# Performance work log

Measured on AMD Instinct MI355X. Metric: run time of the kernel, lower is better.

The kernel has to match this reference:

```python
import jax, jax.numpy as jnp
import numpy as np

EPS = 1e-6
ROPE_THETA = 10000.0
NUM_HEADS = 32
NUM_KV_HEADS = 8
HEAD_DIM = 128
HIDDEN = 4096
B, S = 2, 2048


def setup_inputs() -> dict:
    key = jax.random.key(0)
    ks = jax.random.split(key, 6)
    scale = 0.02
    return {
        "hidden_states": jax.random.normal(ks[0], (B, S, HIDDEN), dtype=jnp.float32),
        "position_ids": jnp.arange(S, dtype=jnp.int64 if jax.config.jax_enable_x64 else jnp.int32)[None, :],
        "Wq": jax.random.normal(ks[1], (HIDDEN, NUM_HEADS * HEAD_DIM), dtype=jnp.float32) * scale,
        "Wk": jax.random.normal(ks[2], (HIDDEN, NUM_KV_HEADS * HEAD_DIM), dtype=jnp.float32) * scale,
        "Wv": jax.random.normal(ks[3], (HIDDEN, NUM_KV_HEADS * HEAD_DIM), dtype=jnp.float32) * scale,
        "Wo": jax.random.normal(ks[4], (NUM_HEADS * HEAD_DIM, HIDDEN), dtype=jnp.float32) * scale,
        "q_norm_w": jnp.ones((HEAD_DIM,), dtype=jnp.float32),
        "k_norm_w": jnp.ones((HEAD_DIM,), dtype=jnp.float32),
    }


def _rms_norm(x, w):
    # RMSNorm over last dim (head_dim)
    var = jnp.mean(jnp.square(x), axis=-1, keepdims=True)
    return x * jax.lax.rsqrt(var + EPS) * w


def _rope(x, position_ids):
    # x: [B, H, S, D]; Llama-style half-split rotation
    d = x.shape[-1]
    inv_freq = 1.0 / (ROPE_THETA ** (jnp.arange(0, d, 2, dtype=jnp.float32) / d))  # [D/2]
    ang = position_ids[:, :, None].astype(jnp.float32) * inv_freq[None, None, :]   # [B, S, D/2]
    emb = jnp.concatenate([ang, ang], axis=-1)                                     # [B, S, D]
    cos = jnp.cos(emb)[:, None, :, :]
    sin = jnp.sin(emb)[:, None, :, :]
    x1, x2 = x[..., : d // 2], x[..., d // 2:]
    rot = jnp.concatenate([-x2, x1], axis=-1)
    return x * cos + rot * sin


def reference(hidden_states, position_ids, Wq, Wk, Wv, Wo, q_norm_w, k_norm_w):
    b, s, _ = hidden_states.shape
    q = (hidden_states @ Wq).reshape(b, s, NUM_HEADS, HEAD_DIM).transpose(0, 2, 1, 3)
    k = (hidden_states @ Wk).reshape(b, s, NUM_KV_HEADS, HEAD_DIM).transpose(0, 2, 1, 3)
    v = (hidden_states @ Wv).reshape(b, s, NUM_KV_HEADS, HEAD_DIM).transpose(0, 2, 1, 3)

    q = _rms_norm(q, q_norm_w)
    k = _rms_norm(k, k_norm_w)

    q = _rope(q, position_ids)
    k = _rope(k, position_ids)

    groups = NUM_HEADS // NUM_KV_HEADS
    k = jnp.repeat(k, groups, axis=1)  # repeat_interleave along head dim
    v = jnp.repeat(v, groups, axis=1)

    scale = 1.0 / jnp.sqrt(jnp.float32(HEAD_DIM))
    scores = jnp.einsum("bhqd,bhkd->bhqk", q, k) * scale
    causal = jnp.tril(jnp.ones((s, s), dtype=bool))
    scores = jnp.where(causal[None, None], scores, jnp.finfo(scores.dtype).min)
    attn = jax.nn.softmax(scores, axis=-1)
    out = jnp.einsum("bhqk,bhkd->bhqd", attn, v)
    out = out.transpose(0, 2, 1, 3).reshape(b, s, NUM_HEADS * HEAD_DIM)
    return out @ Wo
```

## Files before the change

kernel.cpp:

```cpp
#include <hip/hip_runtime.h>
#include <stdint.h>
#include <stddef.h>

#define S_LEN 2048
#define BATCH 2
#define NHEADS 32
#define NKV 8
#define HD 128
#define HIDDEN 4096
#define T_TOK (BATCH * S_LEN)
#define QKV_W 6144

typedef unsigned short u16;
typedef __attribute__((ext_vector_type(4))) float f32x4;
typedef __attribute__((ext_vector_type(16))) float f32x16;
typedef __attribute__((ext_vector_type(8))) short s16x8;
typedef __attribute__((ext_vector_type(4))) unsigned short u16x4;
typedef __attribute__((ext_vector_type(4))) unsigned int u32x4;

__device__ __forceinline__ u16 f2bf(float f) {
  unsigned int u = __builtin_bit_cast(unsigned int, f);
  unsigned int r = (u + 0x7FFFu + ((u >> 16) & 1u)) >> 16;
  return (u16)r;
}
__device__ __forceinline__ float bf2f(u16 h) {
  return __builtin_bit_cast(float, ((unsigned int)h) << 16);
}

__device__ __forceinline__ void gload16(const void* g, void* l) {
  __builtin_amdgcn_global_load_lds((__attribute__((address_space(1))) void*)g,
                                   (__attribute__((address_space(3))) void*)l,
                                   16, 0, 0);
}

__device__ __forceinline__ unsigned cvtpk(float a, float b) {
  unsigned r;
  asm("v_cvt_pk_bf16_f32 %0, %1, %2" : "=v"(r) : "v"(a), "v"(b));
  return r;
}
__device__ __forceinline__ void lohi_dup(unsigned W, unsigned& lo, unsigned& hi) {
  unsigned a = W, b = W;
  asm volatile("v_permlane32_swap_b32 %0, %1" : "+v"(a), "+v"(b));
  lo = a; hi = b;
}

__global__ __launch_bounds__(256) void k_convert(const float* __restrict__ in,
                                                 u16* __restrict__ out, int n8) {
  int i = blockIdx.x * 256 + threadIdx.x;
  if (i >= n8) return;
  float4 a = ((const float4*)in)[i * 2];
  float4 b = ((const float4*)in)[i * 2 + 1];
  u16x4 lo = {f2bf(a.x), f2bf(a.y), f2bf(a.z), f2bf(a.w)};
  u16x4 hi = {f2bf(b.x), f2bf(b.y), f2bf(b.z), f2bf(b.w)};
  ((u16x4*)out)[i * 2] = lo;
  ((u16x4*)out)[i * 2 + 1] = hi;
}

__global__ __launch_bounds__(256) void k_transpose_w(const float* __restrict__ W,
                                                     u16* __restrict__ Wt, int K,
                                                     int N, int outRowOff,
                                                     int outStride) {
  __shared__ float tl[32][33];
  int k0 = blockIdx.x * 32, n0 = blockIdx.y * 32;
  int t = threadIdx.x;
  int r = t >> 3, c4 = (t & 7) * 4;
  float4 v = *(const float4*)&W[(size_t)(k0 + r) * N + n0 + c4];
  tl[r][c4] = v.x; tl[r][c4 + 1] = v.y; tl[r][c4 + 2] = v.z; tl[r][c4 + 3] = v.w;
  __syncthreads();
  u16x4 o = {f2bf(tl[c4][r]), f2bf(tl[c4 + 1][r]), f2bf(tl[c4 + 2][r]),
             f2bf(tl[c4 + 3][r])};
  *(u16x4*)&Wt[(size_t)(outRowOff + n0 + r) * outStride + k0 + c4] = o;
}

__global__ __launch_bounds__(256) void k_rope_tab(const int* __restrict__ pos,
                                                  float* __restrict__ tab) {
  int i = blockIdx.x * 256 + threadIdx.x;
  int s = i >> 6, l = i & 63;
  float p = (float)pos[s];
  float ang = p * expf(-(float)l * 0.14391156516342163f);
  tab[s * 128 + l] = cosf(ang);
  tab[s * 128 + 64 + l] = sinf(ang);
}

template <typename OutT>
__global__ __launch_bounds__(256, 2) void k_gemm128(const u16* __restrict__ A,
                                                    const u16* __restrict__ Bt,
                                                    OutT* __restrict__ C,
                                                    int N, int K) {
  __shared__ u16 As[2][8192];
  __shared__ u16 Bs[2][8192];
  int nbn = N >> 7;
  int nwg = gridDim.x;
  int orig = blockIdx.x;
  int q8 = nwg >> 3, r8 = nwg & 7;
  int xcd = orig & 7, sub = orig >> 3;
  int wgid = (xcd < r8 ? xcd * (q8 + 1) : r8 * (q8 + 1) + (xcd - r8) * q8) + sub;
  int bm = wgid / nbn, bn = wgid % nbn;
  int tid = threadIdx.x, wid = tid >> 6, lane = tid & 63;
  int wm = wid >> 1, wn = wid & 1;
  int g = lane >> 4, c = lane & 15;
  int l3 = lane >> 3, l7 = lane & 7;
  int swz = c & 7;
  int xunit = (l7 ^ l3) * 8;

  f32x4 acc[4][4];
#pragma unroll
  for (int m = 0; m < 4; m++)
#pragma unroll
    for (int n = 0; n < 4; n++) acc[m][n] = (f32x4){0.f, 0.f, 0.f, 0.f};

  const u16* aBase = A + (size_t)(bm * 128 + wid * 32 + l3) * K + xunit;
  const u16* bBase = Bt + (size_t)(bn * 128 + wid * 32 + l3) * K + xunit;

  auto stgA = [&](int buf, int j, size_t koff) {
    gload16(aBase + (size_t)(j * 8) * K + koff, &As[buf][(wid * 32 + j * 8) * 64]);
  };
  auto stgB = [&](int buf, int j, size_t koff) {
    gload16(bBase + (size_t)(j * 8) * K + koff, &Bs[buf][(wid * 32 + j * 8) * 64]);
  };

  int nt = K >> 6;
#pragma unroll
  for (int j = 0; j < 4; j++) { stgA(0, j, 0); stgB(0, j, 0); }
  __syncthreads();

  for (int t = 0; t < nt; t++) {
    int cb = t & 1;
    const u16* Ab = &As[cb][0];
    const u16* Bb = &Bs[cb][0];
    bool s1 = (t + 1 < nt);
    size_t k1 = (size_t)(t + 1) << 6;

    s16x8 af[4][2], bf[4][2];
#pragma unroll
    for (int mi = 0; mi < 4; mi++)
#pragma unroll
      for (int ks = 0; ks < 2; ks++)
        af[mi][ks] = *(const s16x8*)&Ab[(wm * 64 + mi * 16 + c) * 64 +
                                        (((ks * 4 + g) ^ swz) * 8)];
#pragma unroll
    for (int nj = 0; nj < 4; nj++)
#pragma unroll
      for (int ks = 0; ks < 2; ks++)
        bf[nj][ks] = *(const s16x8*)&Bb[(wn * 64 + nj * 16 + c) * 64 +
                                        (((ks * 4 + g) ^ swz) * 8)];
    if (s1) {
#pragma unroll
      for (int j = 0; j < 4; j++) { stgA(cb ^ 1, j, k1); stgB(cb ^ 1, j, k1); }
    }
    __builtin_amdgcn_s_setprio(1);
#pragma unroll
    for (int mi = 0; mi < 4; mi++)
#pragma unroll
      for (int nj = 0; nj < 4; nj++)
#pragma unroll
        for (int ks = 0; ks < 2; ks++)
          acc[mi][nj] = __builtin_amdgcn_mfma_f32_16x16x32_bf16(
              af[mi][ks], bf[nj][ks], acc[mi][nj], 0, 0, 0);
    __builtin_amdgcn_s_setprio(0);
    __syncthreads();
  }

#pragma unroll
  for (int m = 0; m < 4; m++)
#pragma unroll
    for (int n = 0; n < 4; n++) {
      size_t row = (size_t)bm * 128 + wm * 64 + m * 16 + g * 4;
      size_t col = (size_t)bn * 128 + wn * 64 + n * 16 + c;
#pragma unroll
      for (int r = 0; r < 4; r++) {
        float v = acc[m][n][r];
        if constexpr (sizeof(OutT) == 2)
          C[(row + r) * N + col] = (OutT)f2bf(v);
        else
          C[(row + r) * N + col] = (OutT)v;
      }
    }
}

__global__ __launch_bounds__(256) void k_rmsrope(u16* __restrict__ QK,
                                                 const float* __restrict__ w,
                                                 const float* __restrict__ tab,
                                                 int H, int rowStride) {
  int row = blockIdx.x * 4 + (threadIdx.x >> 6);
  int lane = threadIdx.x & 63;
  int t = row / H, h = row - t * H;
  int s = t & (S_LEN - 1);
  u16* p = QK + (size_t)t * rowStride + h * HD;
  float x1 = bf2f(p[lane]), x2 = bf2f(p[lane + 64]);
  float ss = x1 * x1 + x2 * x2;
#pragma unroll
  for (int o = 32; o >= 1; o >>= 1) ss += __shfl_xor(ss, o);
  float inv = rsqrtf(ss * (1.0f / 128.0f) + 1e-6f);
  float y1 = x1 * inv * w[lane], y2 = x2 * inv * w[lane + 64];
  float cs = tab[s * 128 + lane], sn = tab[s * 128 + 64 + lane];
  p[lane] = f2bf(y1 * cs - y2 * sn);
  p[lane + 64] = f2bf(y2 * cs + y1 * sn);
}

__global__ __launch_bounds__(256) void k_transpose_v(const u16* __restrict__ QKV,
                                                     u16* __restrict__ Vt) {
  __shared__ u16 tl[32][40];
  int bkh = blockIdx.x;
  int s0 = blockIdx.y * 32, d0 = blockIdx.z * 32;
  int b = bkh >> 3, kh = bkh & 7;
  int t = threadIdx.x, r = t >> 3, c4 = (t & 7) * 4;
  const u16* src =
      QKV + (size_t)(b * S_LEN + s0 + r) * QKV_W + 5120 + kh * HD + d0 + c4;
  u16x4 v = *(const u16x4*)src;
  tl[r][c4] = v[0]; tl[r][c4 + 1] = v[1]; tl[r][c4 + 2] = v[2]; tl[r][c4 + 3] = v[3];
  __syncthreads();
  u16x4 o = {tl[c4][r], tl[c4 + 1][r], tl[c4 + 2][r], tl[c4 + 3][r]};
  *(u16x4*)&Vt[(size_t)(bkh * HD + d0 + r) * S_LEN + s0 + c4] = o;
}

__global__ __launch_bounds__(256) void k_attn(const u16* __restrict__ QKV,
                                              const u16* __restrict__ Vt,
                                              u16* __restrict__ Oact) {
  __shared__ u16 Ks[2][64 * 128];
  __shared__ u16 Vs[2][128 * 64];
  int bid = blockIdx.x;
  int xcd = bid & 7, slot = bid >> 3;
  int grp = xcd * 2 + (slot >> 5);
  int b = grp >> 3, kh = grp & 7;
  int s32 = slot & 31;
  int pr = s32 >> 2;
  int h = kh * 4 + (s32 & 3);
  int w = threadIdx.x >> 6, lane = threadIdx.x & 63;
  int q31 = lane & 31, hh = lane >> 5;
  const float qscale = 0.12751740810f;

  const char* Kg = (const char*)(QKV + (size_t)b * S_LEN * QKV_W + 4096 + kh * HD);
  const char* Vg = (const char*)(Vt + (size_t)(b * 8 + kh) * HD * S_LEN);

#pragma unroll 1
  for (int half = 0; half < 2; half++) {
    __syncthreads();
    int qt = half ? 15 - pr : pr;
    int qw0 = qt * 128 + w * 32;

    s16x8 qf[8];
    const u16* Qp = QKV + (size_t)(b * S_LEN + qw0 + q31) * QKV_W + h * HD + hh * 8;
#pragma unroll
    for (int dc = 0; dc < 8; dc++) {
      s16x8 raw = *(const s16x8*)(Qp + dc * 16);
#pragma unroll
      for (int e = 0; e < 8; e++)
        qf[dc][e] = (short)f2bf(bf2f((u16)raw[e]) * qscale);
    }

    f32x16 o[4];
#pragma unroll
    for (int d = 0; d < 4; d++)
#pragma unroll
      for (int r = 0; r < 16; r++) o[d][r] = 0.f;
    float m = -3.0e38f, l = 0.f;

    int nch = 2 * qt + 2;

    {
      char* KsB = (char*)Ks[0];
      char* VsB = (char*)Vs[0];
#pragma unroll
      for (int j = 0; j < 4; j++) {
        int ins = w * 4 + j;
        int row = ins * 4 + (lane >> 4);
        int bc = ((lane & 15) * 16) ^ ((row & 7) << 4);
        gload16(Kg + (size_t)row * 12288 + bc, KsB + ins * 1024);
      }
#pragma unroll
      for (int j = 0; j < 4; j++) {
        int ins = w * 4 + j;
        int row = ins * 8 + (lane >> 3);
        int bc = ((lane & 7) * 16) ^ ((row & 7) << 4);
        gload16(Vg + (size_t)row * 4096 + bc, VsB + ins * 1024);
      }
    }

    int cur = 0;
    for (int ch = 0; ch < nch; ch++) {
      int kb = ch * 64;
      __syncthreads();
      if (ch + 1 < nch) {
        char* KsB = (char*)Ks[cur ^ 1];
        char* VsB = (char*)Vs[cur ^ 1];
        int kb2 = kb + 64;
#pragma unroll
        for (int j = 0; j < 4; j++) {
          int ins = w * 4 + j;
          int row = ins * 4 + (lane >> 4);
          int bc = ((lane & 15) * 16) ^ ((row & 7) << 4);
          gload16(Kg + (size_t)(kb2 + row) * 12288 + bc, KsB + ins * 1024);
        }
#pragma unroll
        for (int j = 0; j < 4; j++) {
          int ins = w * 4 + j;
          int row = ins * 8 + (lane >> 3);
          int bc = ((lane & 7) * 16) ^ ((row & 7) << 4);
          gload16(Vg + (size_t)row * 4096 + (size_t)kb2 * 2 + bc, VsB + ins * 1024);
        }
      }
      if (kb <= qw0 + 31) {
        char* KsB = (char*)Ks[cur];
        char* VsB = (char*)Vs[cur];
        f32x16 sA, sB;
#pragma unroll
        for (int r = 0; r < 16; r++) { sA[r] = 0.f; sB[r] = 0.f; }
        int sw = (q31 & 7) << 4;
        __builtin_amdgcn_s_setprio(1);
#pragma unroll
        for (int dc = 0; dc < 8; dc++) {
          s16x8 kfA = *(const s16x8*)(KsB + q31 * 256 + ((dc * 32 + hh * 16) ^ sw));
          s16x8 kfB = *(const s16x8*)(KsB + (32 + q31) * 256 + ((dc * 32 + hh * 16) ^ sw));
          sA = __builtin_amdgcn_mfma_f32_32x32x16_bf16(kfA, qf[dc], sA, 0, 0, 0);
          sB = __builtin_amdgcn_mfma_f32_32x32x16_bf16(kfB, qf[dc], sB, 0, 0, 0);
        }
        __builtin_amdgcn_s_setprio(0);
        if (kb + 63 > qw0) {
          int qa = qw0 + q31;
#pragma unroll
          for (int r = 0; r < 16; r++) {
            int krow = (r & 3) + 8 * (r >> 2) + 4 * hh;
            if (kb + krow > qa) sA[r] = -1e30f;
            if (kb + 32 + krow > qa) sB[r] = -1e30f;
          }
        }
        float mx = -3.0e38f;
#pragma unroll
        for (int r = 0; r < 16; r++) mx = fmaxf(mx, fmaxf(sA[r], sB[r]));
        mx = fmaxf(mx, __shfl_xor(mx, 32));
        if (!__all(mx - m <= 11.5f)) {
          float mnew = fmaxf(m, mx);
          float corr = __builtin_amdgcn_exp2f(m - mnew);
          l *= corr;
#pragma unroll
          for (int d = 0; d < 4; d++)
#pragma unroll
            for (int r = 0; r < 16; r++) o[d][r] *= corr;
          m = mnew;
        }
        float rs = 0.f;
#pragma unroll
        for (int r = 0; r < 16; r++) {
          sA[r] = __builtin_amdgcn_exp2f(sA[r] - m); rs += sA[r];
          sB[r] = __builtin_amdgcn_exp2f(sB[r] - m); rs += sB[r];
        }
        rs += __shfl_xor(rs, 32);
        l += rs;
#pragma unroll
        for (int st = 0; st < 2; st++) {
          unsigned Aw[8], Bw[8];
#pragma unroll
          for (int j = 0; j < 8; j++) {
            float p0 = st ? sB[2 * j] : sA[2 * j];
            float p1 = st ? sB[2 * j + 1] : sA[2 * j + 1];
            lohi_dup(cvtpk(p0, p1), Aw[j], Bw[j]);
          }
#pragma unroll
          for (int kc2 = 0; kc2 < 2; kc2++) {
            u32x4 wv;
            wv.x = hh ? Aw[kc2 * 4 + 2] : Aw[kc2 * 4 + 0];
            wv.y = hh ? Aw[kc2 * 4 + 3] : Aw[kc2 * 4 + 1];
            wv.z = hh ? Bw[kc2 * 4 + 2] : Bw[kc2 * 4 + 0];
            wv.w = hh ? Bw[kc2 * 4 + 3] : Bw[kc2 * 4 + 1];
            s16x8 pf = __builtin_bit_cast(s16x8, wv);
            int kc = st * 2 + kc2;
            __builtin_amdgcn_s_setprio(1);
#pragma unroll
            for (int d = 0; d < 4; d++) {
              int row = d * 32 + q31;
              int vsw = (row & 7) << 4;
              s16x8 vf = *(const s16x8*)(VsB + row * 128 + ((kc * 32 + hh * 16) ^ vsw));
              o[d] = __builtin_amdgcn_mfma_f32_32x32x16_bf16(vf, pf, o[d], 0, 0, 0);
            }
            __builtin_amdgcn_s_setprio(0);
          }
        }
      }
      cur ^= 1;
    }
    float linv = 1.0f / l;
    u16* Op = Oact + (size_t)(b * S_LEN + qw0 + q31) * 4096 + h * HD;
#pragma unroll
    for (int d = 0; d < 4; d++)
#pragma unroll
      for (int g4 = 0; g4 < 4; g4++) {
        int d0 = d * 32 + 8 * g4 + 4 * hh;
        u16x4 w4 = {f2bf(o[d][4 * g4 + 0] * linv), f2bf(o[d][4 * g4 + 1] * linv),
                    f2bf(o[d][4 * g4 + 2] * linv), f2bf(o[d][4 * g4 + 3] * linv)};
        *(u16x4*)(Op + d0) = w4;
      }
  }
}

extern "C" void kernel_launch(void* const* d_in, const int* in_sizes, int n_in,
                              void* d_out, int out_size, void* d_ws,
                              size_t ws_size, hipStream_t stream) {
  (void)in_sizes; (void)n_in; (void)out_size; (void)ws_size;
  const float* X = (const float*)d_in[0];
  const int* pos = (const int*)d_in[1];
  const float* Wq = (const float*)d_in[2];
  const float* Wk = (const float*)d_in[3];
  const float* Wv = (const float*)d_in[4];
  const float* Wo = (const float*)d_in[5];
  const float* qw = (const float*)d_in[6];
  const float* kw = (const float*)d_in[7];
  float* out = (float*)d_out;
  char* ws = (char*)d_ws;

  const size_t MB = 1024ull * 1024ull;
  u16* Xb    = (u16*)(ws + 0 * MB);
  u16* WqkvT = (u16*)(ws + 32 * MB);
  u16* WkvT  = (u16*)(ws + 64 * MB);
  u16* WoT   = (u16*)(ws + 80 * MB);
  u16* QKV   = (u16*)(ws + 112 * MB);
  u16* Vt    = (u16*)(ws + 160 * MB);
  u16* Oact  = (u16*)(ws + 168 * MB);
  float* tab = (float*)(ws + 200 * MB);

  k_convert<<<8192, 256, 0, stream>>>(X, Xb, (T_TOK * HIDDEN) / 8);
  k_transpose_w<<<dim3(128, 128), 256, 0, stream>>>(Wq, WqkvT, 4096, 4096, 0, 4096);
  k_transpose_w<<<dim3(128, 32), 256, 0, stream>>>(Wk, WkvT, 4096, 1024, 0, 4096);
  k_transpose_w<<<dim3(128, 32), 256, 0, stream>>>(Wv, WkvT, 4096, 1024, 1024, 4096);
  k_transpose_w<<<dim3(128, 128), 256, 0, stream>>>(Wo, WoT, 4096, 4096, 0, 4096);
  k_rope_tab<<<512, 256, 0, stream>>>(pos, tab);

  k_gemm128<u16><<<32 * 48, 256, 0, stream>>>(Xb, WqkvT, QKV, QKV_W, 4096);

  k_rmsrope<<<(T_TOK * NHEADS) / 4, 256, 0, stream>>>(QKV, qw, tab, NHEADS, QKV_W);
  k_rmsrope<<<(T_TOK * NKV) / 4, 256, 0, stream>>>(QKV + 4096, kw, tab, NKV, QKV_W);

  k_transpose_v<<<dim3(16, 64, 4), 256, 0, stream>>>(QKV, Vt);

  k_attn<<<512, 256, 0, stream>>>(QKV, Vt, Oact);

  k_gemm128<float><<<32 * 32, 256, 0, stream>>>(Oact, WoT, out, 4096, 4096);
}
```

Measured before the change: 658.8 us.

## Replace 128x128 GEMM with 256x256 8-wave ping-pong pipelined kernel

The bf16 GEMM goes from a 128x128 tile with 4 waves to a 256x256 tile with 8 waves (512 threads). The main loop becomes a hand-scheduled pipeline: each K-tile is split into quadrants, and LDS reads, global-to-LDS loads and MFMA blocks are interleaved under explicit barriers and vmcnt/lgkmcnt waits. The aim is more data reuse per tile and better overlap of memory traffic with MFMA for the QKV and output projections. In exchange the grid is much smaller (384 and 256 workgroups), the kernel uses 128KB of LDS and more accumulator registers, and the manual waitcnt scheduling is fragile.

```diff
diff --git a/kernel.cpp b/kernel.cpp
--- a/kernel.cpp
+++ b/kernel.cpp
@@ -83,13 +83,13 @@
 }
 
 template <typename OutT>
-__global__ __launch_bounds__(256, 2) void k_gemm128(const u16* __restrict__ A,
-                                                    const u16* __restrict__ Bt,
-                                                    OutT* __restrict__ C,
-                                                    int N, int K) {
-  __shared__ u16 As[2][8192];
-  __shared__ u16 Bs[2][8192];
-  int nbn = N >> 7;
+__global__ __launch_bounds__(512, 2) void k_gemm8p(const u16* __restrict__ A,
+                                                   const u16* __restrict__ Bt,
+                                                   OutT* __restrict__ C,
+                                                   int N, int K) {
+  __shared__ u16 As[2][16384];
+  __shared__ u16 Bs[2][16384];
+  int nbn = N >> 8;
   int nwg = gridDim.x;
   int orig = blockIdx.x;
   int q8 = nwg >> 3, r8 = nwg & 7;
@@ -97,76 +97,130 @@
   int wgid = (xcd < r8 ? xcd * (q8 + 1) : r8 * (q8 + 1) + (xcd - r8) * q8) + sub;
   int bm = wgid / nbn, bn = wgid % nbn;
   int tid = threadIdx.x, wid = tid >> 6, lane = tid & 63;
-  int wm = wid >> 1, wn = wid & 1;
+  int wm = wid >> 2, wn = wid & 3;
   int g = lane >> 4, c = lane & 15;
   int l3 = lane >> 3, l7 = lane & 7;
   int swz = c & 7;
   int xunit = (l7 ^ l3) * 8;
 
-  f32x4 acc[4][4];
-#pragma unroll
-  for (int m = 0; m < 4; m++)
+  f32x4 acc[8][4];
+#pragma unroll
+  for (int m = 0; m < 8; m++)
 #pragma unroll
     for (int n = 0; n < 4; n++) acc[m][n] = (f32x4){0.f, 0.f, 0.f, 0.f};
 
-  const u16* aBase = A + (size_t)(bm * 128 + wid * 32 + l3) * K + xunit;
-  const u16* bBase = Bt + (size_t)(bn * 128 + wid * 32 + l3) * K + xunit;
-
-  auto stgA = [&](int buf, int j, size_t koff) {
-    gload16(aBase + (size_t)(j * 8) * K + koff, &As[buf][(wid * 32 + j * 8) * 64]);
+  const u16* aBase = A + (size_t)(bm * 256 + wid * 16 + l3) * K + xunit;
+  const u16* bBase = Bt + (size_t)(bn * 256 + wid * 16 + l3) * K + xunit;
+
+  auto stgA = [&](int buf, int h, size_t koff) {
+    gload16(aBase + (size_t)(h * 128) * K + koff,
+            &As[buf][(h * 128 + wid * 16) * 64]);
+    gload16(aBase + (size_t)(h * 128 + 8) * K + koff,
+            &As[buf][(h * 128 + wid * 16 + 8) * 64]);
   };
-  auto stgB = [&](int buf, int j, size_t koff) {
-    gload16(bBase + (size_t)(j * 8) * K + koff, &Bs[buf][(wid * 32 + j * 8) * 64]);
+  auto stgB = [&](int buf, int h, size_t koff) {
+    gload16(bBase + (size_t)(h * 128) * K + koff,
+            &Bs[buf][(h * 128 + wid * 16) * 64]);
+    gload16(bBase + (size_t)(h * 128 + 8) * K + koff,
+            &Bs[buf][(h * 128 + wid * 16 + 8) * 64]);
   };
 
-  int nt = K >> 6;
-#pragma unroll
-  for (int j = 0; j < 4; j++) { stgA(0, j, 0); stgB(0, j, 0); }
-  __syncthreads();
-
-  for (int t = 0; t < nt; t++) {
-    int cb = t & 1;
-    const u16* Ab = &As[cb][0];
-    const u16* Bb = &Bs[cb][0];
-    bool s1 = (t + 1 < nt);
-    size_t k1 = (size_t)(t + 1) << 6;
-
-    s16x8 af[4][2], bf[4][2];
+  s16x8 af[4][2], bf0[2][2], bf1[2][2];
+  auto rdA = [&](int buf, int mh) {
 #pragma unroll
     for (int mi = 0; mi < 4; mi++)
 #pragma unroll
       for (int ks = 0; ks < 2; ks++)
-        af[mi][ks] = *(const s16x8*)&Ab[(wm * 64 + mi * 16 + c) * 64 +
-                                        (((ks * 4 + g) ^ swz) * 8)];
-#pragma unroll
-    for (int nj = 0; nj < 4; nj++)
+        af[mi][ks] = *(const s16x8*)&As[buf][(wm * 128 + mh * 64 + mi * 16 + c) * 64 +
+                                            (((ks * 4 + g) ^ swz) * 8)];
+  };
+  auto rdB = [&](int buf, int nh, s16x8 (&bf)[2][2]) {
+#pragma unroll
+    for (int nj = 0; nj < 2; nj++)
 #pragma unroll
       for (int ks = 0; ks < 2; ks++)
-        bf[nj][ks] = *(const s16x8*)&Bb[(wn * 64 + nj * 16 + c) * 64 +
-                                        (((ks * 4 + g) ^ swz) * 8)];
-    if (s1) {
-#pragma unroll
-      for (int j = 0; j < 4; j++) { stgA(cb ^ 1, j, k1); stgB(cb ^ 1, j, k1); }
-    }
+        bf[nj][ks] = *(const s16x8*)&Bs[buf][(wn * 64 + nh * 32 + nj * 16 + c) * 64 +
+                                            (((ks * 4 + g) ^ swz) * 8)];
+  };
+  auto quad = [&](int mh, int nh, s16x8 (&bf)[2][2]) {
     __builtin_amdgcn_s_setprio(1);
 #pragma unroll
     for (int mi = 0; mi < 4; mi++)
 #pragma unroll
-      for (int nj = 0; nj < 4; nj++)
+      for (int nj = 0; nj < 2; nj++)
 #pragma unroll
         for (int ks = 0; ks < 2; ks++)
-          acc[mi][nj] = __builtin_amdgcn_mfma_f32_16x16x32_bf16(
-              af[mi][ks], bf[nj][ks], acc[mi][nj], 0, 0, 0);
+          acc[mh * 4 + mi][nh * 2 + nj] = __builtin_amdgcn_mfma_f32_16x16x32_bf16(
+              af[mi][ks], bf[nj][ks], acc[mh * 4 + mi][nh * 2 + nj], 0, 0, 0);
     __builtin_amdgcn_s_setprio(0);
-    __syncthreads();
+  };
+#define BAR() __builtin_amdgcn_s_barrier()
+#define LGKM0() asm volatile("s_waitcnt lgkmcnt(0)" ::: "memory")
+#define VM(n) asm volatile("s_waitcnt vmcnt(" #n ")" ::: "memory")
+
+  int nt2 = K >> 7;
+  stgB(0, 0, 0); stgB(0, 1, 0);
+  stgA(0, 0, 0); stgA(0, 1, 0);
+  stgB(1, 0, 64); stgB(1, 1, 64);
+  VM(4);
+  BAR();
+
+  for (int j = 0; j < nt2; j++) {
+    size_t k1 = (size_t)(2 * j + 1) << 6;
+    size_t k2 = (size_t)(2 * j + 2) << 6;
+    size_t k3 = (size_t)(2 * j + 3) << 6;
+    bool st = (j + 1 < nt2);
+    rdA(0, 0); rdB(0, 0, bf0);
+    stgA(1, 0, k1);
+    BAR(); LGKM0();
+    quad(0, 0, bf0);
+    BAR();
+    rdB(0, 1, bf1);
+    stgA(1, 1, k1);
+    BAR(); LGKM0();
+    quad(0, 1, bf1);
+    BAR();
+    rdA(0, 1);
+    if (st) stgB(0, 0, k2);
+    BAR(); LGKM0();
+    quad(1, 0, bf0);
+    BAR();
+    if (st) stgB(0, 1, k2);
+    BAR(); LGKM0();
+    quad(1, 1, bf1);
+    if (st) { VM(4); } else { VM(0); }
+    BAR();
+    rdA(1, 0); rdB(1, 0, bf0);
+    if (st) stgA(0, 0, k2);
+    BAR(); LGKM0();
+    quad(0, 0, bf0);
+    BAR();
+    rdB(1, 1, bf1);
+    if (st) stgA(0, 1, k2);
+    BAR(); LGKM0();
+    quad(0, 1, bf1);
+    BAR();
+    rdA(1, 1);
+    if (st) stgB(1, 0, k3);
+    BAR(); LGKM0();
+    quad(1, 0, bf0);
+    BAR();
+    if (st) stgB(1, 1, k3);
+    BAR(); LGKM0();
+    quad(1, 1, bf1);
+    if (st) { VM(4); }
+    BAR();
   }
-
-#pragma unroll
-  for (int m = 0; m < 4; m++)
+#undef BAR
+#undef LGKM0
+#undef VM
+
+#pragma unroll
+  for (int m = 0; m < 8; m++)
 #pragma unroll
     for (int n = 0; n < 4; n++) {
-      size_t row = (size_t)bm * 128 + wm * 64 + m * 16 + g * 4;
-      size_t col = (size_t)bn * 128 + wn * 64 + n * 16 + c;
+      size_t row = (size_t)bm * 256 + wm * 128 + m * 16 + g * 4;
+      size_t col = (size_t)bn * 256 + wn * 64 + n * 16 + c;
 #pragma unroll
       for (int r = 0; r < 4; r++) {
         float v = acc[m][n][r];
@@ -425,7 +479,7 @@
   k_transpose_w<<<dim3(128, 128), 256, 0, stream>>>(Wo, WoT, 4096, 4096, 0, 4096);
   k_rope_tab<<<512, 256, 0, stream>>>(pos, tab);
 
-  k_gemm128<u16><<<32 * 48, 256, 0, stream>>>(Xb, WqkvT, QKV, QKV_W, 4096);
+  k_gemm8p<u16><<<16 * 24, 512, 0, stream>>>(Xb, WqkvT, QKV, QKV_W, 4096);
 
   k_rmsrope<<<(T_TOK * NHEADS) / 4, 256, 0, stream>>>(QKV, qw, tab, NHEADS, QKV_W);
   k_rmsrope<<<(T_TOK * NKV) / 4, 256, 0, stream>>>(QKV + 4096, kw, tab, NKV, QKV_W);
@@ -434,5 +488,5 @@
 
   k_attn<<<512, 256, 0, stream>>>(QKV, Vt, Oact);
 
-  k_gemm128<float><<<32 * 32, 256, 0, stream>>>(Oact, WoT, out, 4096, 4096);
-}
+  k_gemm8p<float><<<16 * 16, 512, 0, stream>>>(Oact, WoT, out, 4096, 4096);
+}
```

New measurement: 643.2 us. 1.02x faster.
